# Kernel optimization log

Measured on AMD Instinct MI355X. Metric: run time of the kernel, lower is better.

The kernel has to match this reference:

```python
import jax, jax.numpy as jnp
import numpy as np

N_NODES = 20000
NUM_STEPS = 6
SIGNS = (1.0, -1.0, 1.0, -1.0, 1.0, -1.0)  # TF_POS, TF_NEG, PPI_POS, PPI_NEG, UNDIR, MIRNA_NEG


def setup_inputs() -> dict:
    key = jax.random.key(0)
    ks = jax.random.split(key, 12)
    B, N, E, H, C = 64, N_NODES, 400000, 64, 32
    return {
        "ctl_base": jax.random.normal(ks[0], (B, N), jnp.float32),
        "u_raw": jax.random.normal(ks[1], (B, N), jnp.float32),
        "cell_idx": jax.random.randint(ks[2], (B,), 0, C, jnp.int32),
        "edge_src": jax.random.randint(ks[3], (6, E), 0, N, jnp.int32),
        "edge_dst": jax.random.randint(ks[4], (6, E), 0, N, jnp.int32),
        "edge_val": jax.random.uniform(ks[5], (6, E), jnp.float32),
        "g_logits": jnp.zeros((6,), jnp.float32),
        "alpha_logits": jnp.zeros((NUM_STEPS,), jnp.float32),
        "cell_emb": jax.random.normal(ks[6], (C, H), jnp.float32),
        "W1": jax.random.normal(ks[7], (3, H), jnp.float32) * 0.1,
        "b1": jnp.zeros((H,), jnp.float32),
        "W2": jax.random.normal(ks[8], (H, 1), jnp.float32) * 0.1,
        "b2": jnp.zeros((1,), jnp.float32),
    }


def _spmm_right(h, src, dst, val):
    # out[b, j] = sum_{e: dst[e]==j} h[b, src[e]] * val[e]   (== h @ A)
    gathered = h.T[src] * val[:, None]  # [E, B]
    return jax.ops.segment_sum(gathered, dst, num_segments=N_NODES).T  # [B, N]


def reference(ctl_base, u_raw, g_logits, alpha_logits, cell_emb,
              W1, b1, W2, b2, edge_val, edge_src, edge_dst, cell_idx):
    g = jax.nn.softplus(g_logits)          # [6] relation gates
    alphas = jax.nn.sigmoid(alpha_logits)  # [num_steps]
    h0 = u_raw
    h = u_raw
    for k in range(NUM_STEPS):
        msg = jnp.zeros_like(h)
        for r in range(6):
            msg = msg + SIGNS[r] * g[r] * _spmm_right(h, edge_src[r], edge_dst[r], edge_val[r])
        a = alphas[k]
        h = a * h0 + (1.0 - a) * msg
    # decode: stack [ctl, u_raw, hK] -> [B, N, 3]
    x = jnp.stack([ctl_base, u_raw, h], axis=-1)
    hd = jax.nn.relu(jnp.einsum('bnf,fh->bnh', x, W1) + b1)  # [B, N, H]
    hd = hd + cell_emb[cell_idx][:, None, :]
    y = (jnp.einsum('bnh,ho->bno', hd, W2) + b2)[..., 0]  # [B, N]
    return y
```

## Files before the change

kernel.cpp:

```cpp
#include <hip/hip_runtime.h>

#define N_NODES 20000
#define HID 64
#define NSTEPS 6
#define NSLICE 8
#define SLICE_SZ (N_NODES / NSLICE)
#define SUBB 64
#define NBLK (NSLICE * SUBB)
#define TBLK ((N_NODES + 63) / 64)
#define NB1 512
#define CBLK ((N_NODES + 255) / 256)
#define MAGIC 13422

typedef _Float16 h8_t __attribute__((ext_vector_type(8)));
typedef unsigned u4_t __attribute__((ext_vector_type(4)));

union U16H { unsigned short u; _Float16 h; };
union U4H8 { uint4 u; _Float16 h[8]; };

__device__ __forceinline__ _Float16 us_as_h(unsigned short s) { U16H u; u.u = s; return u.h; }
__device__ __forceinline__ unsigned short h_as_us(_Float16 h) { U16H u; u.h = h; return u.u; }

__device__ __forceinline__ int slice_of(int d) {
    return (int)(((unsigned)d * (unsigned)MAGIC) >> 25);
}
__device__ __forceinline__ float softplusf_(float x) {
    return (x > 0.f) ? (x + log1pf(expf(-x))) : log1pf(expf(x));
}
__device__ __forceinline__ float sigmoidf_(float x) {
    return 1.f / (1.f + expf(-x));
}

__global__ __launch_bounds__(256) void count8_kernel(const int* __restrict__ edst,
                                                     int* __restrict__ gcnt, int TE,
                                                     u4_t* __restrict__ egq, long long egq_n) {
    u4_t z = {0u, 0u, 0u, 0u};
    for (long long i = (long long)blockIdx.x * 256 + threadIdx.x; i < egq_n;
         i += (long long)NB1 * 256)
        __builtin_nontemporal_store(z, egq + i);

    __shared__ int lh[8];
    int bk = blockIdx.x;
    int lane = threadIdx.x & 63;
    if (threadIdx.x < 8) lh[threadIdx.x] = 0;
    __syncthreads();
    int chunk = ((TE + NB1 - 1) / NB1 + 255) & ~255;
    int lo = bk * chunk;
    int hi = min(lo + chunk, TE);
    int my = 0;
    for (int ii = 0; ii < chunk; ii += 256) {
        int i = lo + ii + (int)threadIdx.x;
        bool act = i < hi;
        int s = -1;
        if (act) s = slice_of(__builtin_nontemporal_load(edst + i));
#pragma unroll
        for (int q = 0; q < 8; ++q) {
            unsigned long long b = __ballot(s == q);
            if (lane == q) my += (int)__popcll(b);
        }
    }
    if (lane < 8) atomicAdd(&lh[lane], my);
    __syncthreads();
    if (threadIdx.x < 8) gcnt[bk * 8 + threadIdx.x] = lh[threadIdx.x];
}

__global__ __launch_bounds__(256) void scan8_kernel(const int* __restrict__ gcnt,
                                                    int* __restrict__ blkoff,
                                                    int* __restrict__ bbase,
                                                    const float* __restrict__ g_logits,
                                                    const float* __restrict__ alpha_logits,
                                                    const int* __restrict__ cell_idx,
                                                    const float* __restrict__ cell_emb,
                                                    const float* __restrict__ W2,
                                                    const float* __restrict__ b2,
                                                    float* __restrict__ gsign,
                                                    float* __restrict__ alph,
                                                    float* __restrict__ cell_dot) {
    __shared__ int psum[8][33];
    int tid = threadIdx.x;
    int s = tid >> 5, g = tid & 31;
    const int per = NB1 / 32;
    int sum = 0;
    for (int b = g * per; b < (g + 1) * per; ++b) sum += gcnt[b * 8 + s];
    psum[s][g] = sum;
    __syncthreads();
    if (tid < 8) {
        int run = 0;
        for (int i = 0; i < 32; ++i) { int v = psum[tid][i]; psum[tid][i] = run; run += v; }
        psum[tid][32] = run;
    }
    __syncthreads();
    int run = psum[s][g];
    for (int b = g * per; b < (g + 1) * per; ++b) {
        blkoff[b * 8 + s] = run;
        run += gcnt[b * 8 + s];
    }
    if (tid == 0) {
        int acc = 0;
        bbase[0] = 0;
        for (int q = 0; q < 8; ++q) { acc += psum[q][32]; bbase[q + 1] = acc; }
    }
    if (tid < 64) {
        if (tid < 6) gsign[tid] = ((tid & 1) ? -1.f : 1.f) * softplusf_(g_logits[tid]);
        if (tid < NSTEPS) alph[tid] = sigmoidf_(alpha_logits[tid]);
        int ci = cell_idx[tid];
        float acc = b2[0];
        for (int hh = 0; hh < HID; ++hh) acc = fmaf(cell_emb[ci * HID + hh], W2[hh], acc);
        cell_dot[tid] = acc;
    }
}

__global__ __launch_bounds__(256) void bucket_kernel(const int* __restrict__ esrc,
                                                     const int* __restrict__ edst,
                                                     const float* __restrict__ eval,
                                                     const float* __restrict__ gsign,
                                                     const int* __restrict__ blkoff,
                                                     const int* __restrict__ bbase,
                                                     int2* __restrict__ bucket,
                                                     int E, int TE) {
    __shared__ int lcur[8];
    int bk = blockIdx.x;
    int lane = threadIdx.x & 63;
    if (threadIdx.x < 8) lcur[threadIdx.x] = bbase[threadIdx.x] + blkoff[bk * 8 + threadIdx.x];
    __syncthreads();
    int chunk = ((TE + NB1 - 1) / NB1 + 255) & ~255;
    int lo = bk * chunk;
    int hi = min(lo + chunk, TE);
    for (int ii = 0; ii < chunk; ii += 256) {
        int i = lo + ii + (int)threadIdx.x;
        bool act = i < hi;
        int s = -1, meta = 0, cb = 0;
        if (act) {
            int d  = __builtin_nontemporal_load(edst + i);
            int sv = __builtin_nontemporal_load(esrc + i);
            float ev = __builtin_nontemporal_load(eval + i);
            s = slice_of(d);
            int dl = d - s * SLICE_SZ;
            meta = sv | (dl << 16);
            int r = (i >= E) + (i >= 2 * E) + (i >= 3 * E) + (i >= 4 * E) + (i >= 5 * E);
            cb = __float_as_int(gsign[r] * ev);
        }
        int pos = 0;
#pragma unroll
        for (int q = 0; q < 8; ++q) {
            unsigned long long b = __ballot(s == q);
            if (b) {
                int leader = (int)__ffsll(b) - 1;
                int base = 0;
                if (lane == leader) base = atomicAdd(&lcur[q], (int)__popcll(b));
                base = __shfl(base, leader);
                if (s == q) pos = base + (int)__popcll(b & ((1ull << lane) - 1ull));
            }
        }
        if (act) bucket[pos] = make_int2(meta, cb);
    }
}

__global__ __launch_bounds__(256) void hist2db_kernel(const int2* __restrict__ bucket,
                                                      const int* __restrict__ bbase,
                                                      int* __restrict__ blkcnt) {
    __shared__ int lh[SLICE_SZ];
    int bk = blockIdx.x;
    int slice = bk & (NSLICE - 1);
    int sub = bk >> 3;
    for (int b = threadIdx.x; b < SLICE_SZ; b += 256) lh[b] = 0;
    __syncthreads();
    int lo = bbase[slice];
    int total = bbase[slice + 1] - lo;
    int chunk = ((total + SUBB - 1) / SUBB + 255) & ~255;
    int beg = lo + sub * chunk;
    int end = min(beg + chunk, lo + total);
    const int* mp = (const int*)bucket;
    for (int i = beg + (int)threadIdx.x; i < end; i += 256) {
        int meta = __builtin_nontemporal_load(mp + 2 * (size_t)i);
        atomicAdd(&lh[((unsigned)meta) >> 16], 1);
    }
    __syncthreads();
    int* out = blkcnt + (size_t)(slice * SUBB + sub) * SLICE_SZ;
    for (int b = threadIdx.x; b < SLICE_SZ; b += 256) out[b] = lh[b];
}

__global__ __launch_bounds__(256) void colscan_kernel(int* __restrict__ blkcnt,
                                                      int* __restrict__ counts,
                                                      int* __restrict__ blksum) {
    int n = blockIdx.x * 256 + threadIdx.x;
    int run = 0;
    if (n < N_NODES) {
        int slice = n / SLICE_SZ, bin = n % SLICE_SZ;
        size_t base = (size_t)slice * SUBB * SLICE_SZ + bin;
#pragma unroll 8
        for (int s = 0; s < SUBB; ++s) {
            size_t idx = base + (size_t)s * SLICE_SZ;
            int t = blkcnt[idx];
            blkcnt[idx] = run;
            run += t;
        }
        counts[n] = run;
    }
    int g = (n < N_NODES) ? ((run + 7) >> 3) : 0;
#pragma unroll
    for (int st = 1; st < 64; st <<= 1) g += __shfl_xor(g, st, 64);
    __shared__ int wsum[4];
    if ((threadIdx.x & 63) == 0) wsum[threadIdx.x >> 6] = g;
    __syncthreads();
    if (threadIdx.x == 0) blksum[blockIdx.x] = wsum[0] + wsum[1] + wsum[2] + wsum[3];
}

__global__ __launch_bounds__(256) void scan2_kernel(const int* __restrict__ counts,
                                                    const int* __restrict__ blksum,
                                                    int* __restrict__ grp_ptr, int n) {
    int b = blockIdx.x;
    int tid = threadIdx.x, lane = tid & 63, wid = tid >> 6;
    int i = b * 256 + tid;
    int v = (i < n) ? ((counts[i] + 7) >> 3) : 0;
    int x = v;
#pragma unroll
    for (int st = 1; st < 64; st <<= 1) {
        int t = __shfl_up(x, st, 64);
        if (lane >= st) x += t;
    }
    __shared__ int wsum[4];
    if (lane == 63) wsum[wid] = x;
    int s = ((lane < b) ? blksum[lane] : 0) +
            ((lane + 64 < b) ? blksum[lane + 64] : 0);
#pragma unroll
    for (int st = 1; st < 64; st <<= 1) s += __shfl_xor(s, st, 64);
    __syncthreads();
    int woff = s;
    if (wid > 0) woff += wsum[0];
    if (wid > 1) woff += wsum[1];
    if (wid > 2) woff += wsum[2];
    int off = woff + x - v;
    if (i < n) grp_ptr[i] = off;
    if (i == n - 1) grp_ptr[n] = off + v;
}

__global__ __launch_bounds__(256) void scatter2b_kernel(const int2* __restrict__ bucket,
                                                        const int* __restrict__ bbase,
                                                        const int* __restrict__ grp_ptr,
                                                        const int* __restrict__ blkcnt,
                                                        unsigned* __restrict__ eg,
                                                        const float* __restrict__ u_raw,
                                                        float* __restrict__ u_t,
                                                        _Float16* __restrict__ uh) {
    __shared__ float smem[64 * 65];
    int bk = blockIdx.x;
    if (bk >= NBLK) {
        float(*tile)[65] = (float(*)[65])smem;
        int c0 = (bk - NBLK) * 64;
        int tx = threadIdx.x & 63, ty = threadIdx.x >> 6;
#pragma unroll
        for (int i = 0; i < 16; ++i) {
            int c = c0 + tx;
            tile[ty + i * 4][tx] = (c < N_NODES) ? u_raw[(size_t)(ty + i * 4) * N_NODES + c] : 0.f;
        }
        __syncthreads();
#pragma unroll
        for (int i = 0; i < 16; ++i) {
            int c = c0 + ty + i * 4;
            if (c < N_NODES) {
                float v = tile[tx][ty + i * 4];
                u_t[(size_t)c * 64 + tx] = v;
                uh[(size_t)c * 64 + tx] = (_Float16)v;
            }
        }
        return;
    }
    int* lbase = (int*)smem;
    int slice = bk & (NSLICE - 1);
    int sub = bk >> 3;
    int lo_n = slice * SLICE_SZ;
    const int* boff = blkcnt + (size_t)(slice * SUBB + sub) * SLICE_SZ;
    for (int b = threadIdx.x; b < SLICE_SZ; b += 256)
        lbase[b] = grp_ptr[lo_n + b] * 8 + boff[b];
    __syncthreads();
    int lo = bbase[slice];
    int total = bbase[slice + 1] - lo;
    int chunk = ((total + SUBB - 1) / SUBB + 255) & ~255;
    int beg = lo + sub * chunk;
    int end = min(beg + chunk, lo + total);
    for (int i = beg + (int)threadIdx.x; i < end; i += 256) {
        long long rec = __builtin_nontemporal_load((const long long*)bucket + i);
        int meta = (int)rec;
        float cf = __int_as_float((int)(rec >> 32));
        int pos = atomicAdd(&lbase[((unsigned)meta) >> 16], 1);
        eg[pos] = (unsigned)(meta & 0xFFFF) | ((unsigned)h_as_us((_Float16)cf) << 16);
    }
}

__global__ __launch_bounds__(256) void step_kernel(const _Float16* __restrict__ h_in,
                                                   const float* __restrict__ h0,
                                                   _Float16* __restrict__ h_out,
                                                   float* __restrict__ hF,
                                                   const int* __restrict__ grp_ptr,
                                                   const unsigned* __restrict__ eg,
                                                   const float* __restrict__ alph,
                                                   int k, int last) {
    int lane = threadIdx.x & 63;
    int node = blockIdx.x * 4 + (threadIdx.x >> 6);
    if (node >= N_NODES) return;
    int gb = __builtin_amdgcn_readfirstlane(grp_ptr[node]);
    int ge = __builtin_amdgcn_readfirstlane(grp_ptr[node + 1]);
    int sub8 = lane >> 3;
    const _Float16* hbase = h_in + (lane & 7) * 8;
    float acc[8] = {0.f, 0.f, 0.f, 0.f, 0.f, 0.f, 0.f, 0.f};
    int g = gb;
    for (; g + 2 <= ge; g += 2) {
        unsigned e0 = eg[(size_t)g * 8 + sub8];
        unsigned e1 = eg[(size_t)g * 8 + 8 + sub8];
        h8_t v0 = *(const h8_t*)(hbase + (e0 & 0xFFFFu) * 64);
        h8_t v1 = *(const h8_t*)(hbase + (e1 & 0xFFFFu) * 64);
        float c0 = (float)us_as_h((unsigned short)(e0 >> 16));
        float c1 = (float)us_as_h((unsigned short)(e1 >> 16));
#pragma unroll
        for (int j = 0; j < 8; ++j) acc[j] = fmaf((float)v0[j], c0, acc[j]);
#pragma unroll
        for (int j = 0; j < 8; ++j) acc[j] = fmaf((float)v1[j], c1, acc[j]);
    }
    if (g < ge) {
        unsigned e0 = eg[(size_t)g * 8 + sub8];
        h8_t v0 = *(const h8_t*)(hbase + (e0 & 0xFFFFu) * 64);
        float c0 = (float)us_as_h((unsigned short)(e0 >> 16));
#pragma unroll
        for (int j = 0; j < 8; ++j) acc[j] = fmaf((float)v0[j], c0, acc[j]);
    }
#pragma unroll
    for (int st = 8; st < 64; st <<= 1) {
#pragma unroll
        for (int j = 0; j < 8; ++j) acc[j] += __shfl_xor(acc[j], st, 64);
    }
    if (lane < 8) {
        float a = alph[k];
        int base = node * 64 + lane * 8;
        float4 h0a = *(const float4*)(h0 + base);
        float4 h0b = *(const float4*)(h0 + base + 4);
        float om = 1.f - a;
        float r0 = fmaf(a, h0a.x, om * acc[0]);
        float r1 = fmaf(a, h0a.y, om * acc[1]);
        float r2 = fmaf(a, h0a.z, om * acc[2]);
        float r3 = fmaf(a, h0a.w, om * acc[3]);
        float r4 = fmaf(a, h0b.x, om * acc[4]);
        float r5 = fmaf(a, h0b.y, om * acc[5]);
        float r6 = fmaf(a, h0b.z, om * acc[6]);
        float r7 = fmaf(a, h0b.w, om * acc[7]);
        if (last) {
            *(float4*)(hF + base)     = make_float4(r0, r1, r2, r3);
            *(float4*)(hF + base + 4) = make_float4(r4, r5, r6, r7);
        } else {
            U4H8 o;
            o.h[0] = (_Float16)r0; o.h[1] = (_Float16)r1;
            o.h[2] = (_Float16)r2; o.h[3] = (_Float16)r3;
            o.h[4] = (_Float16)r4; o.h[5] = (_Float16)r5;
            o.h[6] = (_Float16)r6; o.h[7] = (_Float16)r7;
            *(uint4*)(h_out + base) = o.u;
        }
    }
}

__global__ __launch_bounds__(256) void decode_kernel(float* __restrict__ y,
                                                     const float* __restrict__ ctl,
                                                     const float* __restrict__ u,
                                                     const float* __restrict__ hF,
                                                     const float* __restrict__ W1,
                                                     const float* __restrict__ b1,
                                                     const float* __restrict__ W2,
                                                     const float* __restrict__ cell_dot) {
    __shared__ float tile[64][65];
    __shared__ float4 pack[HID];
    __shared__ float w2s[HID];
    __shared__ float cds[64];
    if (threadIdx.x < HID) {
        int hh = threadIdx.x;
        pack[hh] = make_float4(W1[0 * HID + hh], W1[1 * HID + hh], W1[2 * HID + hh], b1[hh]);
        w2s[hh] = W2[hh];
        cds[hh] = cell_dot[hh];
    }
    int n0 = blockIdx.x * 64;
    int tx = threadIdx.x & 63, ty = threadIdx.x >> 6;
#pragma unroll
    for (int i = 0; i < 16; ++i) {
        int n = n0 + ty + i * 4;
        tile[ty + i * 4][tx] = (n < N_NODES) ? hF[(size_t)n * 64 + tx] : 0.f;
    }
    __syncthreads();
#pragma unroll
    for (int i = 0; i < 16; ++i) {
        int b = ty + i * 4;
        int n = n0 + tx;
        if (n < N_NODES) {
            size_t idx = (size_t)b * N_NODES + n;
            float xc = ctl[idx], xu = u[idx], xh = tile[tx][b];
            float acc = 0.f;
#pragma unroll 8
            for (int hh = 0; hh < HID; ++hh) {
                float4 p = pack[hh];
                float t = fmaf(xc, p.x, fmaf(xu, p.y, fmaf(xh, p.z, p.w)));
                t = fmaxf(t, 0.f);
                acc = fmaf(t, w2s[hh], acc);
            }
            y[idx] = acc + cds[b];
        }
    }
}

extern "C" void kernel_launch(void* const* d_in, const int* in_sizes, int n_in,
                              void* d_out, int out_size, void* d_ws, size_t ws_size,
                              hipStream_t stream) {
    const float* ctl          = (const float*)d_in[0];
    const float* u_raw        = (const float*)d_in[1];
    const int*   cell_idx     = (const int*)d_in[2];
    const int*   edge_src     = (const int*)d_in[3];
    const int*   edge_dst     = (const int*)d_in[4];
    const float* edge_val     = (const float*)d_in[5];
    const float* g_logits     = (const float*)d_in[6];
    const float* alpha_logits = (const float*)d_in[7];
    const float* cell_emb     = (const float*)d_in[8];
    const float* W1           = (const float*)d_in[9];
    const float* b1           = (const float*)d_in[10];
    const float* W2           = (const float*)d_in[11];
    const float* b2           = (const float*)d_in[12];
    float* y = (float*)d_out;

    const int TE = in_sizes[3];
    const int E  = TE / 6;
    const int NB = N_NODES * 64;

    char* ws = (char*)d_ws;
    size_t off = 0;
    auto alloc = [&](size_t bytes) -> char* {
        char* p = ws + off;
        off += (bytes + 255) & ~(size_t)255;
        return p;
    };
    int* grp_ptr = (int*)alloc((N_NODES + 1) * sizeof(int));
    int* counts  = (int*)alloc(N_NODES * sizeof(int));
    int* blksum  = (int*)alloc(CBLK * sizeof(int));
    int* blkcnt  = (int*)alloc((size_t)NSLICE * SUBB * SLICE_SZ * sizeof(int));
    int* gcnt    = (int*)alloc((size_t)NB1 * 8 * sizeof(int));
    int* blkoff  = (int*)alloc((size_t)NB1 * 8 * sizeof(int));
    int* bbase   = (int*)alloc(16 * sizeof(int));
    const size_t MAXG = (size_t)TE / 8 + N_NODES + 8;
    unsigned* eg = (unsigned*)alloc(MAXG * 8 * sizeof(unsigned));
    int2* bucket    = (int2*)alloc((size_t)TE * sizeof(int2));
    _Float16* uh    = (_Float16*)alloc((size_t)NB * 2);
    _Float16* hA    = (_Float16*)alloc((size_t)NB * 2);
    _Float16* hB    = (_Float16*)alloc((size_t)NB * 2);
    float* hF       = (float*)alloc((size_t)NB * 4);
    float* u_t      = (float*)alloc((size_t)NB * sizeof(float));
    float* gsign    = (float*)alloc(8 * sizeof(float));
    float* alph     = (float*)alloc(8 * sizeof(float));
    float* cell_dot = (float*)alloc(64 * sizeof(float));

    count8_kernel<<<NB1, 256, 0, stream>>>(edge_dst, gcnt, TE,
                                           (u4_t*)eg, (long long)(MAXG * 2));
    scan8_kernel<<<1, 256, 0, stream>>>(gcnt, blkoff, bbase, g_logits, alpha_logits,
                                        cell_idx, cell_emb, W2, b2,
                                        gsign, alph, cell_dot);
    bucket_kernel<<<NB1, 256, 0, stream>>>(edge_src, edge_dst, edge_val, gsign,
                                           blkoff, bbase, bucket, E, TE);
    hist2db_kernel<<<NBLK, 256, 0, stream>>>(bucket, bbase, blkcnt);
    colscan_kernel<<<CBLK, 256, 0, stream>>>(blkcnt, counts, blksum);
    scan2_kernel<<<CBLK, 256, 0, stream>>>(counts, blksum, grp_ptr, N_NODES);
    scatter2b_kernel<<<NBLK + TBLK, 256, 0, stream>>>(bucket, bbase, grp_ptr, blkcnt,
                                                      eg, u_raw, u_t, uh);

    const _Float16* hin = uh;
    for (int k = 0; k < NSTEPS; ++k) {
        _Float16* hout = (k & 1) ? hB : hA;
        step_kernel<<<(N_NODES + 3) / 4, 256, 0, stream>>>(hin, u_t, hout, hF, grp_ptr,
                                                           eg, alph, k, k == NSTEPS - 1);
        hin = hout;
    }

    decode_kernel<<<TBLK, 256, 0, stream>>>(y, ctl, u_raw, hF, W1, b1, W2, cell_dot);
}
```

Before: 364.9 us.

## Switch propagation state from fp16 to fp32 with 4-edge groups and software pipelining

The intermediate h buffers change from fp16 to fp32. The step kernel now processes 4 edges per group, with 16 lanes each loading a float4, and a software-pipelined loop prefetches edge records and rows two pairs ahead. The edge grouping changes from 8 to 4 per group, and the bucketing/scan grid sizes (SUBB, NB1) grow. This doubles the gather bandwidth per edge in exchange for better latency hiding, removes fp16 conversions and the separate hF buffer, and adds padding overhead for the smaller groups.

```diff
diff --git a/kernel.cpp b/kernel.cpp
--- a/kernel.cpp
+++ b/kernel.cpp
@@ -5,18 +5,17 @@
 #define NSTEPS 6
 #define NSLICE 8
 #define SLICE_SZ (N_NODES / NSLICE)
-#define SUBB 64
+#define SUBB 256
 #define NBLK (NSLICE * SUBB)
 #define TBLK ((N_NODES + 63) / 64)
-#define NB1 512
+#define NB1 2048
 #define CBLK ((N_NODES + 255) / 256)
 #define MAGIC 13422
 
-typedef _Float16 h8_t __attribute__((ext_vector_type(8)));
+typedef float f4_t __attribute__((ext_vector_type(4)));
 typedef unsigned u4_t __attribute__((ext_vector_type(4)));
 
 union U16H { unsigned short u; _Float16 h; };
-union U4H8 { uint4 u; _Float16 h[8]; };
 
 __device__ __forceinline__ _Float16 us_as_h(unsigned short s) { U16H u; u.u = s; return u.h; }
 __device__ __forceinline__ unsigned short h_as_us(_Float16 h) { U16H u; u.h = h; return u.u; }
@@ -197,7 +196,7 @@
         }
         counts[n] = run;
     }
-    int g = (n < N_NODES) ? ((run + 7) >> 3) : 0;
+    int g = (n < N_NODES) ? ((run + 3) >> 2) : 0;
 #pragma unroll
     for (int st = 1; st < 64; st <<= 1) g += __shfl_xor(g, st, 64);
     __shared__ int wsum[4];
@@ -212,7 +211,7 @@
     int b = blockIdx.x;
     int tid = threadIdx.x, lane = tid & 63, wid = tid >> 6;
     int i = b * 256 + tid;
-    int v = (i < n) ? ((counts[i] + 7) >> 3) : 0;
+    int v = (i < n) ? ((counts[i] + 3) >> 2) : 0;
     int x = v;
 #pragma unroll
     for (int st = 1; st < 64; st <<= 1) {
@@ -241,8 +240,7 @@
                                                         const int* __restrict__ blkcnt,
                                                         unsigned* __restrict__ eg,
                                                         const float* __restrict__ u_raw,
-                                                        float* __restrict__ u_t,
-                                                        _Float16* __restrict__ uh) {
+                                                        float* __restrict__ u_t) {
     __shared__ float smem[64 * 65];
     int bk = blockIdx.x;
     if (bk >= NBLK) {
@@ -258,11 +256,7 @@
 #pragma unroll
         for (int i = 0; i < 16; ++i) {
             int c = c0 + ty + i * 4;
-            if (c < N_NODES) {
-                float v = tile[tx][ty + i * 4];
-                u_t[(size_t)c * 64 + tx] = v;
-                uh[(size_t)c * 64 + tx] = (_Float16)v;
-            }
+            if (c < N_NODES) u_t[(size_t)c * 64 + tx] = tile[tx][ty + i * 4];
         }
         return;
     }
@@ -272,7 +266,7 @@
     int lo_n = slice * SLICE_SZ;
     const int* boff = blkcnt + (size_t)(slice * SUBB + sub) * SLICE_SZ;
     for (int b = threadIdx.x; b < SLICE_SZ; b += 256)
-        lbase[b] = grp_ptr[lo_n + b] * 8 + boff[b];
+        lbase[b] = grp_ptr[lo_n + b] * 4 + boff[b];
     __syncthreads();
     int lo = bbase[slice];
     int total = bbase[slice + 1] - lo;
@@ -288,72 +282,84 @@
     }
 }
 
-__global__ __launch_bounds__(256) void step_kernel(const _Float16* __restrict__ h_in,
+__global__ __launch_bounds__(256) void step_kernel(const float* __restrict__ h_in,
                                                    const float* __restrict__ h0,
-                                                   _Float16* __restrict__ h_out,
-                                                   float* __restrict__ hF,
+                                                   float* __restrict__ h_out,
                                                    const int* __restrict__ grp_ptr,
                                                    const unsigned* __restrict__ eg,
                                                    const float* __restrict__ alph,
-                                                   int k, int last) {
+                                                   int k) {
     int lane = threadIdx.x & 63;
     int node = blockIdx.x * 4 + (threadIdx.x >> 6);
     if (node >= N_NODES) return;
     int gb = __builtin_amdgcn_readfirstlane(grp_ptr[node]);
     int ge = __builtin_amdgcn_readfirstlane(grp_ptr[node + 1]);
-    int sub8 = lane >> 3;
-    const _Float16* hbase = h_in + (lane & 7) * 8;
-    float acc[8] = {0.f, 0.f, 0.f, 0.f, 0.f, 0.f, 0.f, 0.f};
+    int sub4 = lane >> 4;
+    const float* hbase = h_in + (lane & 15) * 4;
+    const unsigned* ep = eg + sub4;
+    float acc[4] = {0.f, 0.f, 0.f, 0.f};
     int g = gb;
-    for (; g + 2 <= ge; g += 2) {
-        unsigned e0 = eg[(size_t)g * 8 + sub8];
-        unsigned e1 = eg[(size_t)g * 8 + 8 + sub8];
-        h8_t v0 = *(const h8_t*)(hbase + (e0 & 0xFFFFu) * 64);
-        h8_t v1 = *(const h8_t*)(hbase + (e1 & 0xFFFFu) * 64);
-        float c0 = (float)us_as_h((unsigned short)(e0 >> 16));
-        float c1 = (float)us_as_h((unsigned short)(e1 >> 16));
-#pragma unroll
-        for (int j = 0; j < 8; ++j) acc[j] = fmaf((float)v0[j], c0, acc[j]);
-#pragma unroll
-        for (int j = 0; j < 8; ++j) acc[j] = fmaf((float)v1[j], c1, acc[j]);
-    }
-    if (g < ge) {
-        unsigned e0 = eg[(size_t)g * 8 + sub8];
-        h8_t v0 = *(const h8_t*)(hbase + (e0 & 0xFFFFu) * 64);
-        float c0 = (float)us_as_h((unsigned short)(e0 >> 16));
-#pragma unroll
-        for (int j = 0; j < 8; ++j) acc[j] = fmaf((float)v0[j], c0, acc[j]);
-    }
-#pragma unroll
-    for (int st = 8; st < 64; st <<= 1) {
-#pragma unroll
-        for (int j = 0; j < 8; ++j) acc[j] += __shfl_xor(acc[j], st, 64);
-    }
-    if (lane < 8) {
+    int pairs = (ge - g) >> 1;
+    if (pairs >= 2) {
+        size_t b0 = (size_t)g * 4;
+        unsigned ea0 = ep[b0], ea1 = ep[b0 + 4];
+        f4_t va0 = *(const f4_t*)(hbase + (ea0 & 0xFFFFu) * 64);
+        f4_t va1 = *(const f4_t*)(hbase + (ea1 & 0xFFFFu) * 64);
+        unsigned eb0 = ep[b0 + 8], eb1 = ep[b0 + 12];
+        int p = 0;
+        for (; p + 2 < pairs; ++p) {
+            f4_t vb0 = *(const f4_t*)(hbase + (eb0 & 0xFFFFu) * 64);
+            f4_t vb1 = *(const f4_t*)(hbase + (eb1 & 0xFFFFu) * 64);
+            size_t bn = (size_t)(g + 2 * (p + 2)) * 4;
+            unsigned ec0 = ep[bn], ec1 = ep[bn + 4];
+            float c0 = (float)us_as_h((unsigned short)(ea0 >> 16));
+            float c1 = (float)us_as_h((unsigned short)(ea1 >> 16));
+#pragma unroll
+            for (int j = 0; j < 4; ++j) acc[j] = fmaf(va0[j], c0, acc[j]);
+#pragma unroll
+            for (int j = 0; j < 4; ++j) acc[j] = fmaf(va1[j], c1, acc[j]);
+            ea0 = eb0; ea1 = eb1; eb0 = ec0; eb1 = ec1;
+            va0 = vb0; va1 = vb1;
+        }
+        f4_t vb0 = *(const f4_t*)(hbase + (eb0 & 0xFFFFu) * 64);
+        f4_t vb1 = *(const f4_t*)(hbase + (eb1 & 0xFFFFu) * 64);
+        float c0 = (float)us_as_h((unsigned short)(ea0 >> 16));
+        float c1 = (float)us_as_h((unsigned short)(ea1 >> 16));
+        float c2 = (float)us_as_h((unsigned short)(eb0 >> 16));
+        float c3 = (float)us_as_h((unsigned short)(eb1 >> 16));
+#pragma unroll
+        for (int j = 0; j < 4; ++j) acc[j] = fmaf(va0[j], c0, acc[j]);
+#pragma unroll
+        for (int j = 0; j < 4; ++j) acc[j] = fmaf(va1[j], c1, acc[j]);
+#pragma unroll
+        for (int j = 0; j < 4; ++j) acc[j] = fmaf(vb0[j], c2, acc[j]);
+#pragma unroll
+        for (int j = 0; j < 4; ++j) acc[j] = fmaf(vb1[j], c3, acc[j]);
+        g += 2 * pairs;
+    }
+    for (; g < ge; ++g) {
+        unsigned e = ep[(size_t)g * 4];
+        f4_t v = *(const f4_t*)(hbase + (e & 0xFFFFu) * 64);
+        float c = (float)us_as_h((unsigned short)(e >> 16));
+#pragma unroll
+        for (int j = 0; j < 4; ++j) acc[j] = fmaf(v[j], c, acc[j]);
+    }
+#pragma unroll
+    for (int st = 16; st < 64; st <<= 1) {
+#pragma unroll
+        for (int j = 0; j < 4; ++j) acc[j] += __shfl_xor(acc[j], st, 64);
+    }
+    if (lane < 16) {
         float a = alph[k];
-        int base = node * 64 + lane * 8;
-        float4 h0a = *(const float4*)(h0 + base);
-        float4 h0b = *(const float4*)(h0 + base + 4);
+        int base = node * 64 + lane * 4;
+        float4 h0v = *(const float4*)(h0 + base);
         float om = 1.f - a;
-        float r0 = fmaf(a, h0a.x, om * acc[0]);
-        float r1 = fmaf(a, h0a.y, om * acc[1]);
-        float r2 = fmaf(a, h0a.z, om * acc[2]);
-        float r3 = fmaf(a, h0a.w, om * acc[3]);
-        float r4 = fmaf(a, h0b.x, om * acc[4]);
-        float r5 = fmaf(a, h0b.y, om * acc[5]);
-        float r6 = fmaf(a, h0b.z, om * acc[6]);
-        float r7 = fmaf(a, h0b.w, om * acc[7]);
-        if (last) {
-            *(float4*)(hF + base)     = make_float4(r0, r1, r2, r3);
-            *(float4*)(hF + base + 4) = make_float4(r4, r5, r6, r7);
-        } else {
-            U4H8 o;
-            o.h[0] = (_Float16)r0; o.h[1] = (_Float16)r1;
-            o.h[2] = (_Float16)r2; o.h[3] = (_Float16)r3;
-            o.h[4] = (_Float16)r4; o.h[5] = (_Float16)r5;
-            o.h[6] = (_Float16)r6; o.h[7] = (_Float16)r7;
-            *(uint4*)(h_out + base) = o.u;
-        }
+        float4 r;
+        r.x = fmaf(a, h0v.x, om * acc[0]);
+        r.y = fmaf(a, h0v.y, om * acc[1]);
+        r.z = fmaf(a, h0v.z, om * acc[2]);
+        r.w = fmaf(a, h0v.w, om * acc[3]);
+        *(float4*)(h_out + base) = r;
     }
 }
 
@@ -439,20 +445,18 @@
     int* gcnt    = (int*)alloc((size_t)NB1 * 8 * sizeof(int));
     int* blkoff  = (int*)alloc((size_t)NB1 * 8 * sizeof(int));
     int* bbase   = (int*)alloc(16 * sizeof(int));
-    const size_t MAXG = (size_t)TE / 8 + N_NODES + 8;
-    unsigned* eg = (unsigned*)alloc(MAXG * 8 * sizeof(unsigned));
+    const size_t MAXG = (size_t)TE / 4 + N_NODES + 8;
+    unsigned* eg = (unsigned*)alloc(MAXG * 4 * sizeof(unsigned));
     int2* bucket    = (int2*)alloc((size_t)TE * sizeof(int2));
-    _Float16* uh    = (_Float16*)alloc((size_t)NB * 2);
-    _Float16* hA    = (_Float16*)alloc((size_t)NB * 2);
-    _Float16* hB    = (_Float16*)alloc((size_t)NB * 2);
-    float* hF       = (float*)alloc((size_t)NB * 4);
+    float* hA       = (float*)alloc((size_t)NB * sizeof(float));
+    float* hB       = (float*)alloc((size_t)NB * sizeof(float));
     float* u_t      = (float*)alloc((size_t)NB * sizeof(float));
     float* gsign    = (float*)alloc(8 * sizeof(float));
     float* alph     = (float*)alloc(8 * sizeof(float));
     float* cell_dot = (float*)alloc(64 * sizeof(float));
 
     count8_kernel<<<NB1, 256, 0, stream>>>(edge_dst, gcnt, TE,
-                                           (u4_t*)eg, (long long)(MAXG * 2));
+                                           (u4_t*)eg, (long long)MAXG);
     scan8_kernel<<<1, 256, 0, stream>>>(gcnt, blkoff, bbase, g_logits, alpha_logits,
                                         cell_idx, cell_emb, W2, b2,
                                         gsign, alph, cell_dot);
@@ -462,15 +466,16 @@
     colscan_kernel<<<CBLK, 256, 0, stream>>>(blkcnt, counts, blksum);
     scan2_kernel<<<CBLK, 256, 0, stream>>>(counts, blksum, grp_ptr, N_NODES);
     scatter2b_kernel<<<NBLK + TBLK, 256, 0, stream>>>(bucket, bbase, grp_ptr, blkcnt,
-                                                      eg, u_raw, u_t, uh);
-
-    const _Float16* hin = uh;
+                                                      eg, u_raw, u_t);
+
+    const float* hin = u_t;
+    float* hout = hA;
     for (int k = 0; k < NSTEPS; ++k) {
-        _Float16* hout = (k & 1) ? hB : hA;
-        step_kernel<<<(N_NODES + 3) / 4, 256, 0, stream>>>(hin, u_t, hout, hF, grp_ptr,
-                                                           eg, alph, k, k == NSTEPS - 1);
+        hout = (k & 1) ? hB : hA;
+        step_kernel<<<(N_NODES + 3) / 4, 256, 0, stream>>>(hin, u_t, hout, grp_ptr,
+                                                           eg, alph, k);
         hin = hout;
     }
 
-    decode_kernel<<<TBLK, 256, 0, stream>>>(y, ctl, u_raw, hF, W1, b1, W2, cell_dot);
-}
+    decode_kernel<<<TBLK, 256, 0, stream>>>(y, ctl, u_raw, hout, W1, b1, W2, cell_dot);
+}
```

Result: slower. 439.0 us (+20.3%).
